# Kernel optimization log

Hardware: AMD Instinct MI355X
Metric: run time of the kernel (lower is better)

Reference implementation:

```python
import jax, jax.numpy as jnp
import numpy as np

N_NODES = 40000
N_EDGES = 640000
D = 128
N_GRAPHS = 64


def gcn_conv(x, W, b, edge_index):
    """PyG-style GCNConv: add self-loops, symmetric norm, linear, scatter-add."""
    n = x.shape[0]
    loops = jnp.arange(n, dtype=edge_index.dtype)
    src = jnp.concatenate([edge_index[0], loops])  # message sources (x_j)
    dst = jnp.concatenate([edge_index[1], loops])  # aggregation targets
    # deg computed over targets (col) with unit edge weights, incl. self-loops
    deg = jax.ops.segment_sum(jnp.ones_like(src, dtype=x.dtype), dst, num_segments=n)
    dinv = jnp.where(deg > 0, jax.lax.rsqrt(jnp.maximum(deg, 1.0)), 0.0)
    norm = dinv[src] * dinv[dst]  # [E+N]
    h = x @ W  # [N, d_out]
    out = jax.ops.segment_sum(norm[:, None] * h[src], dst, num_segments=n)
    return out + b


def global_mean_pool(x, batch, num_graphs):
    summed = jax.ops.segment_sum(x, batch, num_segments=num_graphs)
    counts = jax.ops.segment_sum(jnp.ones((x.shape[0],), x.dtype), batch, num_segments=num_graphs)
    return summed / jnp.maximum(counts, 1.0)[:, None]


def setup_inputs() -> dict:
    key = jax.random.key(0)
    ks = jax.random.split(key, 6)
    x = jax.random.normal(ks[0], (N_NODES, D), dtype=jnp.float32)
    edge_index = jax.random.randint(ks[1], (2, N_EDGES), 0, N_NODES)
    batch = jnp.sort(jax.random.randint(ks[2], (N_NODES,), 0, N_GRAPHS))
    s = 1.0 / np.sqrt(D)
    W1 = jax.random.normal(ks[3], (D, D), dtype=jnp.float32) * s
    W2 = jax.random.normal(ks[4], (D, D), dtype=jnp.float32) * s
    b1 = jnp.zeros((D,), jnp.float32)
    b2 = jnp.zeros((D,), jnp.float32)
    return {"x": x, "edge_index": edge_index, "batch": batch,
            "W1": W1, "b1": b1, "W2": W2, "b2": b2}


def reference(x, edge_index, batch, W1, b1, W2, b2):
    h = jax.nn.relu(gcn_conv(x, W1, b1, edge_index))
    h = gcn_conv(h, W2, b2, edge_index)  # no ReLU on last layer
    return global_mean_pool(h, batch, N_GRAPHS)
```

## Files before the change

kernel.cpp:

```cpp
#include <hip/hip_runtime.h>

#define D 128
#define N_GRAPHS 64

typedef unsigned int uint32;
typedef __attribute__((ext_vector_type(8))) _Float16 f16x8;
typedef __attribute__((ext_vector_type(4))) float f32x4;

__device__ __forceinline__ float hl(uint32 u) {
    return (float)__builtin_bit_cast(_Float16, (unsigned short)(u & 0xFFFF));
}
__device__ __forceinline__ float hh(uint32 u) {
    return (float)__builtin_bit_cast(_Float16, (unsigned short)(u >> 16));
}
__device__ __forceinline__ uint32 h2pair(float a, float b) {
    unsigned short ua = __builtin_bit_cast(unsigned short, (_Float16)a);
    unsigned short ub = __builtin_bit_cast(unsigned short, (_Float16)b);
    return (uint32)ua | ((uint32)ub << 16);
}

__global__ __launch_bounds__(256) void prep_kernel(int* __restrict__ cnt,
                                                   const float* __restrict__ W1,
                                                   uint32* __restrict__ Wh, int n) {
    int i = blockIdx.x * 256 + threadIdx.x;
    if (i < n) {
        cnt[i] = 0;
    } else if (i < n + D * (D / 2)) {
        int j = i - n;
        int nn = j & 127, kd = j >> 7;
        float v0 = W1[(size_t)(2 * kd) * D + nn];
        float v1 = W1[(size_t)(2 * kd + 1) * D + nn];
        Wh[nn * 64 + kd] = h2pair(v0, v1);
    }
}


#define GBM 64

__global__ __launch_bounds__(256) void count_gemm_kernel(
    const float* __restrict__ A, const uint32* __restrict__ Wh,
    uint32* __restrict__ hb, int M, int gemmBlocks,
    const int* __restrict__ dst, int* __restrict__ cnt,
    int* __restrict__ rank, int E) {
    __shared__ uint32 lds[64 * 68];

    if (blockIdx.x >= gemmBlocks) {
        int e = (blockIdx.x - gemmBlocks) * 256 + threadIdx.x;
        if (e < E) rank[e] = atomicAdd(&cnt[dst[e]], 1);
        return;
    }

    uint32* As = lds;
    int tid = threadIdx.x;
    int row0 = blockIdx.x * GBM;

#pragma unroll
    for (int j = 0; j < 8; ++j) {
        int idx = tid + j * 256;
        int r = idx >> 5, c4 = idx & 31;
        float4 v = make_float4(0.f, 0.f, 0.f, 0.f);
        if (row0 + r < M) v = *(const float4*)&A[(size_t)(row0 + r) * D + c4 * 4];
        As[r * 68 + c4 * 2 + 0] = h2pair(v.x, v.y);
        As[r * 68 + c4 * 2 + 1] = h2pair(v.z, v.w);
    }
    __syncthreads();

    int wave = tid >> 6, lane = tid & 63;
    int quad = lane >> 4, l16 = lane & 15;
    int wr = (wave & 1) * 32;
    int wc = (wave >> 1) * 64;
    f32x4 acc[2][4];
#pragma unroll
    for (int mi = 0; mi < 2; ++mi)
#pragma unroll
        for (int ni = 0; ni < 4; ++ni) acc[mi][ni] = (f32x4){0.f, 0.f, 0.f, 0.f};

#pragma unroll
    for (int ks = 0; ks < 4; ++ks) {
        int kd = ks * 16 + quad * 4;
        f16x8 a0 = *(f16x8*)&As[(wr + l16) * 68 + kd];
        f16x8 a1 = *(f16x8*)&As[(wr + 16 + l16) * 68 + kd];
        f16x8 b0 = *(const f16x8*)&Wh[(wc + l16) * 64 + kd];
        f16x8 b1 = *(const f16x8*)&Wh[(wc + 16 + l16) * 64 + kd];
        f16x8 b2 = *(const f16x8*)&Wh[(wc + 32 + l16) * 64 + kd];
        f16x8 b3 = *(const f16x8*)&Wh[(wc + 48 + l16) * 64 + kd];
        acc[0][0] = __builtin_amdgcn_mfma_f32_16x16x32_f16(a0, b0, acc[0][0], 0, 0, 0);
        acc[0][1] = __builtin_amdgcn_mfma_f32_16x16x32_f16(a0, b1, acc[0][1], 0, 0, 0);
        acc[0][2] = __builtin_amdgcn_mfma_f32_16x16x32_f16(a0, b2, acc[0][2], 0, 0, 0);
        acc[0][3] = __builtin_amdgcn_mfma_f32_16x16x32_f16(a0, b3, acc[0][3], 0, 0, 0);
        acc[1][0] = __builtin_amdgcn_mfma_f32_16x16x32_f16(a1, b0, acc[1][0], 0, 0, 0);
        acc[1][1] = __builtin_amdgcn_mfma_f32_16x16x32_f16(a1, b1, acc[1][1], 0, 0, 0);
        acc[1][2] = __builtin_amdgcn_mfma_f32_16x16x32_f16(a1, b2, acc[1][2], 0, 0, 0);
        acc[1][3] = __builtin_amdgcn_mfma_f32_16x16x32_f16(a1, b3, acc[1][3], 0, 0, 0);
    }
    __syncthreads();

    unsigned short* cs = (unsigned short*)lds;
#pragma unroll
    for (int mi = 0; mi < 2; ++mi)
#pragma unroll
        for (int ni = 0; ni < 4; ++ni)
#pragma unroll
            for (int r = 0; r < 4; ++r) {
                int row = wr + mi * 16 + quad * 4 + r;
                int col2 = wc + ni * 16 + l16;
                cs[row * 128 + col2] =
                    __builtin_bit_cast(unsigned short, (_Float16)acc[mi][ni][r]);
            }
    __syncthreads();
#pragma unroll
    for (int j = 0; j < 4; ++j) {
        int idx = tid + j * 256;
        int r = idx >> 4, q = idx & 15;
        if (row0 + r < M)
            *(uint4*)&hb[(size_t)(row0 + r) * 64 + q * 4] = *(uint4*)&lds[r * 64 + q * 4];
    }
}


__global__ __launch_bounds__(1024) void scanA_kernel(const int* __restrict__ cnt,
                                                     int* __restrict__ rowptr,
                                                     int* __restrict__ tot,
                                                     float* __restrict__ dinv, int n) {
    __shared__ int swave[16];
    int t = threadIdx.x;
    int lane = t & 63, wave = t >> 6;
    int i = blockIdx.x * 1024 + t;
    int orig = (i < n) ? cnt[i] : 0;
    int v = orig;
#pragma unroll
    for (int off = 1; off < 64; off <<= 1) {
        int u = __shfl_up(v, off, 64);
        if (lane >= off) v += u;
    }
    if (lane == 63) swave[wave] = v;
    __syncthreads();
    if (wave == 0) {
        int wv = (lane < 16) ? swave[lane] : 0;
#pragma unroll
        for (int off = 1; off < 16; off <<= 1) {
            int u = __shfl_up(wv, off, 64);
            if (lane >= off) wv += u;
        }
        if (lane < 16) swave[lane] = wv;
    }
    if (i < n) dinv[i] = rsqrtf((float)(orig + 1));
    __syncthreads();
    int incl = v + ((wave > 0) ? swave[wave - 1] : 0);
    if (i < n) rowptr[i] = incl - orig;
    if (t == 1023) tot[blockIdx.x] = incl;
}

__global__ __launch_bounds__(1024) void scanB_kernel(int* __restrict__ rowptr,
                                                     const int* __restrict__ tot,
                                                     int n, int nchunks) {
    __shared__ int soff;
    int b = blockIdx.x, t = threadIdx.x;
    if (t == 0) {
        int o = 0;
        for (int j = 0; j < b; ++j) o += tot[j];
        soff = o;
    }
    __syncthreads();
    int i = b * 1024 + t;
    if (i < n) rowptr[i] += soff;
    if (b == 0 && t == 0) {
        int o = 0;
        for (int j = 0; j < nchunks; ++j) o += tot[j];
        rowptr[n] = o;
    }
}

__global__ __launch_bounds__(256) void scale_fill_kernel(
    uint32* __restrict__ hb, const float* __restrict__ dinv, int scaleBlocks, int n,
    const int* __restrict__ src, const int* __restrict__ dst,
    const int* __restrict__ rowptr, const int* __restrict__ rank,
    int* __restrict__ col, int E) {
    if (blockIdx.x >= scaleBlocks) {
        int e = (blockIdx.x - scaleBlocks) * 256 + threadIdx.x;
        if (e < E) col[rowptr[dst[e]] + rank[e]] = src[e];
        return;
    }
    int idx = blockIdx.x * 256 + threadIdx.x;
    if (idx < n * 16) {
        int node = idx >> 4;
        float dv = dinv[node];
        uint4 v = ((uint4*)hb)[idx];
        v.x = h2pair(dv * hl(v.x), dv * hh(v.x));
        v.y = h2pair(dv * hl(v.y), dv * hh(v.y));
        v.z = h2pair(dv * hl(v.z), dv * hh(v.z));
        v.w = h2pair(dv * hl(v.w), dv * hh(v.w));
        ((uint4*)hb)[idx] = v;
    }
}


__global__ __launch_bounds__(128) void agg_kernel(const uint32* __restrict__ hb,
                                                  const int* __restrict__ rowptr,
                                                  const int* __restrict__ col,
                                                  const float* __restrict__ dinv,
                                                  const float* __restrict__ bias,
                                                  uint32* __restrict__ h1, int n) {
    int tid = threadIdx.x;
    int lane16 = tid & 15;
    int slot = tid >> 4;
    int node = blockIdx.x * 8 + slot;
    if (node >= n) return;
    const uint4* __restrict__ h4 = (const uint4*)hb;

    float di = dinv[node];
    uint4 su = h4[(size_t)node * 16 + lane16];
    float a0 = hl(su.x), a1 = hh(su.x), a2 = hl(su.y), a3 = hh(su.y);
    float a4 = hl(su.z), a5 = hh(su.z), a6 = hl(su.w), a7 = hh(su.w);

    int k = rowptr[node], end = rowptr[node + 1];
    for (; k + 8 <= end; k += 8) {
        uint4 v[8];
#pragma unroll
        for (int j = 0; j < 8; ++j) v[j] = h4[(size_t)col[k + j] * 16 + lane16];
#pragma unroll
        for (int j = 0; j < 8; ++j) {
            a0 += hl(v[j].x); a1 += hh(v[j].x);
            a2 += hl(v[j].y); a3 += hh(v[j].y);
            a4 += hl(v[j].z); a5 += hh(v[j].z);
            a6 += hl(v[j].w); a7 += hh(v[j].w);
        }
    }
    for (; k < end; ++k) {
        uint4 v = h4[(size_t)col[k] * 16 + lane16];
        a0 += hl(v.x); a1 += hh(v.x);
        a2 += hl(v.y); a3 += hh(v.y);
        a4 += hl(v.z); a5 += hh(v.z);
        a6 += hl(v.w); a7 += hh(v.w);
    }

    float4 b4a = ((const float4*)bias)[2 * lane16];
    float4 b4b = ((const float4*)bias)[2 * lane16 + 1];
    float r0 = fmaxf(fmaf(di, a0, b4a.x), 0.f);
    float r1 = fmaxf(fmaf(di, a1, b4a.y), 0.f);
    float r2 = fmaxf(fmaf(di, a2, b4a.z), 0.f);
    float r3 = fmaxf(fmaf(di, a3, b4a.w), 0.f);
    float r4 = fmaxf(fmaf(di, a4, b4b.x), 0.f);
    float r5 = fmaxf(fmaf(di, a5, b4b.y), 0.f);
    float r6 = fmaxf(fmaf(di, a6, b4b.z), 0.f);
    float r7 = fmaxf(fmaf(di, a7, b4b.w), 0.f);
    uint4 o;
    o.x = h2pair(di * r0, di * r1);
    o.y = h2pair(di * r2, di * r3);
    o.z = h2pair(di * r4, di * r5);
    o.w = h2pair(di * r6, di * r7);
    ((uint4*)h1)[(size_t)node * 16 + lane16] = o;
}


__global__ __launch_bounds__(128) void agg2_kernel(const uint32* __restrict__ h1,
                                                   const int* __restrict__ rowptr,
                                                   const int* __restrict__ col,
                                                   const float* __restrict__ dinv,
                                                   float* __restrict__ P2, int n) {
    int tid = threadIdx.x;
    int lane16 = tid & 15;
    int slot = tid >> 4;
    int node = blockIdx.x * 8 + slot;
    if (node >= n) return;
    const uint4* __restrict__ h4 = (const uint4*)h1;

    float di = dinv[node];
    uint4 su = h4[(size_t)node * 16 + lane16];
    float a0 = hl(su.x), a1 = hh(su.x), a2 = hl(su.y), a3 = hh(su.y);
    float a4 = hl(su.z), a5 = hh(su.z), a6 = hl(su.w), a7 = hh(su.w);

    int k = rowptr[node], end = rowptr[node + 1];
    for (; k + 8 <= end; k += 8) {
        uint4 v[8];
#pragma unroll
        for (int j = 0; j < 8; ++j) v[j] = h4[(size_t)col[k + j] * 16 + lane16];
#pragma unroll
        for (int j = 0; j < 8; ++j) {
            a0 += hl(v[j].x); a1 += hh(v[j].x);
            a2 += hl(v[j].y); a3 += hh(v[j].y);
            a4 += hl(v[j].z); a5 += hh(v[j].z);
            a6 += hl(v[j].w); a7 += hh(v[j].w);
        }
    }
    for (; k < end; ++k) {
        uint4 v = h4[(size_t)col[k] * 16 + lane16];
        a0 += hl(v.x); a1 += hh(v.x);
        a2 += hl(v.y); a3 += hh(v.y);
        a4 += hl(v.z); a5 += hh(v.z);
        a6 += hl(v.w); a7 += hh(v.w);
    }

    float* p = &P2[(size_t)node * D + lane16 * 8];
    *(float4*)&p[0] = make_float4(di * a0, di * a1, di * a2, di * a3);
    *(float4*)&p[4] = make_float4(di * a4, di * a5, di * a6, di * a7);
}

#define PSL 16

__global__ __launch_bounds__(128) void pool_kernel(const float* __restrict__ P2,
                                                   const int* __restrict__ batch,
                                                   float* __restrict__ Ppart, int n) {
    __shared__ int srange[2];
    int t = threadIdx.x;
    int g = blockIdx.x >> 4;
    int kslice = blockIdx.x & 15;
    if (t == 0) {
        int lo = 0, hi = n;
        while (lo < hi) { int mid = (lo + hi) >> 1; if (batch[mid] < g) lo = mid + 1; else hi = mid; }
        srange[0] = lo;
        int g1 = g + 1;
        lo = 0; hi = n;
        while (lo < hi) { int mid = (lo + hi) >> 1; if (batch[mid] < g1) lo = mid + 1; else hi = mid; }
        srange[1] = lo;
    }
    __syncthreads();
    int lb = srange[0], cntg = srange[1] - srange[0];
    int a = lb + (int)(((long long)cntg * kslice) >> 4);
    int b = lb + (int)(((long long)cntg * (kslice + 1)) >> 4);

    float s = 0.f;
    int node = a;
    for (; node + 4 <= b; node += 4) {
        float v0 = P2[(size_t)(node + 0) * D + t];
        float v1 = P2[(size_t)(node + 1) * D + t];
        float v2 = P2[(size_t)(node + 2) * D + t];
        float v3 = P2[(size_t)(node + 3) * D + t];
        s += (v0 + v1) + (v2 + v3);
    }
    for (; node < b; ++node) s += P2[(size_t)node * D + t];
    Ppart[(size_t)blockIdx.x * D + t] = s;
}

__global__ __launch_bounds__(256) void out_kernel(const float* __restrict__ Ppart,
                                                  const float* __restrict__ W2,
                                                  const float* __restrict__ b2,
                                                  const int* __restrict__ batch, int n,
                                                  float* __restrict__ out) {
    __shared__ float gs[D];
    __shared__ float part[2][D];
    __shared__ float srinv;
    int g = blockIdx.x, t = threadIdx.x;
    int f = t & 127, half = t >> 7;
    if (t == 0) {
        int lo = 0, hi = n;
        while (lo < hi) { int mid = (lo + hi) >> 1; if (batch[mid] < g) lo = mid + 1; else hi = mid; }
        int lb = lo;
        int g1 = g + 1;
        lo = 0; hi = n;
        while (lo < hi) { int mid = (lo + hi) >> 1; if (batch[mid] < g1) lo = mid + 1; else hi = mid; }
        int cg = lo - lb;
        srinv = (cg > 0) ? 1.0f / (float)cg : 0.0f;
    }
    float s = 0.f;
    int j0 = half * (PSL / 2);
#pragma unroll
    for (int j = j0; j < j0 + PSL / 2; ++j)
        s += Ppart[((size_t)g * PSL + j) * D + f];
    part[half][f] = s;
    __syncthreads();
    if (half == 0) gs[f] = part[0][f] + part[1][f];
    __syncthreads();
    float acc = 0.f;
    int k0 = half * (D / 2);
#pragma unroll 8
    for (int k = k0; k < k0 + D / 2; ++k) acc = fmaf(gs[k], W2[k * D + f], acc);
    part[half][f] = acc;
    __syncthreads();
    if (half == 0) {
        float a = part[0][f] + part[1][f];
        float r = srinv;
        out[g * D + f] = (r > 0.f) ? fmaf(a, r, b2[f]) : 0.f;
    }
}


extern "C" void kernel_launch(void* const* d_in, const int* in_sizes, int n_in,
                              void* d_out, int out_size, void* d_ws, size_t ws_size,
                              hipStream_t stream) {
    const float* x  = (const float*)d_in[0];
    const int*   ei = (const int*)d_in[1];
    const int*   batch = (const int*)d_in[2];
    const float* W1 = (const float*)d_in[3];
    const float* b1 = (const float*)d_in[4];
    const float* W2 = (const float*)d_in[5];
    const float* b2 = (const float*)d_in[6];
    float* out = (float*)d_out;

    const int n = in_sizes[2];
    const int E = in_sizes[1] / 2;
    const int* src = ei;
    const int* dst = ei + E;

    char* ws = (char*)d_ws;
    size_t off = 0;
    auto carve = [&](size_t bytes) {
        size_t o = off;
        off = (off + bytes + 255) & ~(size_t)255;
        return (void*)(ws + o);
    };
    int*    cnt    = (int*)carve((size_t)n * 4);
    int*    rowptr = (int*)carve((size_t)(n + 1) * 4);
    float*  dinv   = (float*)carve((size_t)n * 4);
    int*    col    = (int*)carve((size_t)E * 4);
    uint32* hb     = (uint32*)carve((size_t)n * D * 2);
    uint32* h1     = (uint32*)carve((size_t)n * D * 2);
    int*    tot    = (int*)carve(64 * 4);
    int*    rank   = (int*)carve((size_t)E * 4);
    uint32* Wh     = (uint32*)carve((size_t)D * (D / 2) * 4);
    float*  P2     = (float*)carve((size_t)n * D * 4);
    float*  Ppart  = (float*)hb;
    (void)ws_size;

    const int nchunks = (n + 1023) >> 10;

    prep_kernel<<<(n + D * (D / 2) + 255) / 256, 256, 0, stream>>>(cnt, W1, Wh, n);

    const int gemmBlocks = (n + GBM - 1) / GBM;
    const int countBlocks = (E + 255) / 256;
    count_gemm_kernel<<<gemmBlocks + countBlocks, 256, 0, stream>>>(
        x, Wh, hb, n, gemmBlocks, dst, cnt, rank, E);

    scanA_kernel<<<nchunks, 1024, 0, stream>>>(cnt, rowptr, tot, dinv, n);
    scanB_kernel<<<nchunks, 1024, 0, stream>>>(rowptr, tot, n, nchunks);
    const int scaleBlocks = (n * 16 + 255) / 256;
    const int fillBlocks = (E + 255) / 256;
    scale_fill_kernel<<<scaleBlocks + fillBlocks, 256, 0, stream>>>(
        hb, dinv, scaleBlocks, n, src, dst, rowptr, rank, col, E);

    agg_kernel<<<(n + 7) / 8, 128, 0, stream>>>(hb, rowptr, col, dinv, b1, h1, n);

    agg2_kernel<<<(n + 7) / 8, 128, 0, stream>>>(h1, rowptr, col, dinv, P2, n);
    pool_kernel<<<N_GRAPHS * PSL, 128, 0, stream>>>(P2, batch, Ppart, n);
    out_kernel<<<N_GRAPHS, 256, 0, stream>>>(Ppart, W2, b2, batch, n, out);
}
```

Baseline: 192.4 us.

## Build CSR with LDS-privatized range histograms instead of global atomics

Replaces the global per-edge atomicAdd counting and rank array with per-block shared-memory histograms over node ranges and edge slices, followed by a column scan that produces per-slice base offsets. The scatter pass reuses LDS atomics to place column indices. The aim is to avoid contended global atomics and the rank buffer traffic. In exchange, each histogram block rereads its full edge slice once per node range (four ranges), so dst is read several times, and a 64-slice partial array plus an extra scan kernel are added.

```diff
diff --git a/kernel.cpp b/kernel.cpp
--- a/kernel.cpp
+++ b/kernel.cpp
@@ -19,15 +19,14 @@
     return (uint32)ua | ((uint32)ub << 16);
 }
 
-__global__ __launch_bounds__(256) void prep_kernel(int* __restrict__ cnt,
-                                                   const float* __restrict__ W1,
-                                                   uint32* __restrict__ Wh, int n) {
+#define BPR 10240
+#define NSLICE 64
+
+__global__ __launch_bounds__(256) void prep_kernel(const float* __restrict__ W1,
+                                                   uint32* __restrict__ Wh) {
     int i = blockIdx.x * 256 + threadIdx.x;
-    if (i < n) {
-        cnt[i] = 0;
-    } else if (i < n + D * (D / 2)) {
-        int j = i - n;
-        int nn = j & 127, kd = j >> 7;
+    if (i < D * (D / 2)) {
+        int nn = i & 127, kd = i >> 7;
         float v0 = W1[(size_t)(2 * kd) * D + nn];
         float v1 = W1[(size_t)(2 * kd + 1) * D + nn];
         Wh[nn * 64 + kd] = h2pair(v0, v1);
@@ -37,16 +36,30 @@
 
 #define GBM 64
 
-__global__ __launch_bounds__(256) void count_gemm_kernel(
+__global__ __launch_bounds__(256) void hist_gemm_kernel(
     const float* __restrict__ A, const uint32* __restrict__ Wh,
     uint32* __restrict__ hb, int M, int gemmBlocks,
-    const int* __restrict__ dst, int* __restrict__ cnt,
-    int* __restrict__ rank, int E) {
-    __shared__ uint32 lds[64 * 68];
+    const int* __restrict__ dst, uint32* __restrict__ partial,
+    int n, int E, int esl) {
+    __shared__ uint32 lds[BPR];
 
     if (blockIdx.x >= gemmBlocks) {
-        int e = (blockIdx.x - gemmBlocks) * 256 + threadIdx.x;
-        if (e < E) rank[e] = atomicAdd(&cnt[dst[e]], 1);
+        int hid = blockIdx.x - gemmBlocks;
+        int r = hid / NSLICE, s = hid % NSLICE;
+        int tid = threadIdx.x;
+#pragma unroll
+        for (int i = tid; i < BPR; i += 256) lds[i] = 0;
+        __syncthreads();
+        int bin0 = r * BPR;
+        int bin1 = min(bin0 + BPR, n);
+        int e0 = s * esl, e1 = min(e0 + esl, E);
+        for (int e = e0 + tid; e < e1; e += 256) {
+            int d = dst[e];
+            if (d >= bin0 && d < bin1) atomicAdd(&lds[d - bin0], 1u);
+        }
+        __syncthreads();
+        for (int i = tid; i < bin1 - bin0; i += 256)
+            partial[(size_t)s * n + bin0 + i] = lds[i];
         return;
     }
 
@@ -117,6 +130,21 @@
     }
 }
 
+__global__ __launch_bounds__(1024) void colscan_kernel(uint32* __restrict__ partial,
+                                                       int* __restrict__ cnt, int n) {
+    int bin = blockIdx.x * 1024 + threadIdx.x;
+    if (bin >= n) return;
+    uint32 run = 0;
+#pragma unroll 8
+    for (int s = 0; s < NSLICE; ++s) {
+        size_t idx = (size_t)s * n + bin;
+        uint32 v = partial[idx];
+        partial[idx] = run;
+        run += v;
+    }
+    cnt[bin] = (int)run;
+}
+
 
 __global__ __launch_bounds__(1024) void scanA_kernel(const int* __restrict__ cnt,
                                                      int* __restrict__ rowptr,
@@ -171,17 +199,32 @@
     }
 }
 
-__global__ __launch_bounds__(256) void scale_fill_kernel(
-    uint32* __restrict__ hb, const float* __restrict__ dinv, int scaleBlocks, int n,
+__global__ __launch_bounds__(256) void scatter_scale_kernel(
+    uint32* __restrict__ hb, const float* __restrict__ dinv, int scatBlocks, int n,
     const int* __restrict__ src, const int* __restrict__ dst,
-    const int* __restrict__ rowptr, const int* __restrict__ rank,
-    int* __restrict__ col, int E) {
-    if (blockIdx.x >= scaleBlocks) {
-        int e = (blockIdx.x - scaleBlocks) * 256 + threadIdx.x;
-        if (e < E) col[rowptr[dst[e]] + rank[e]] = src[e];
+    const int* __restrict__ rowptr, const uint32* __restrict__ base,
+    int* __restrict__ col, int E, int esl) {
+    __shared__ uint32 run[BPR];
+    if (blockIdx.x < scatBlocks) {
+        int r = blockIdx.x / NSLICE, s = blockIdx.x % NSLICE;
+        int tid = threadIdx.x;
+#pragma unroll
+        for (int i = tid; i < BPR; i += 256) run[i] = 0;
+        __syncthreads();
+        int bin0 = r * BPR;
+        int bin1 = min(bin0 + BPR, n);
+        int e0 = s * esl, e1 = min(e0 + esl, E);
+        for (int e = e0 + tid; e < e1; e += 256) {
+            int d = dst[e];
+            if (d >= bin0 && d < bin1) {
+                uint32 lr = atomicAdd(&run[d - bin0], 1u);
+                int pos = rowptr[d] + (int)base[(size_t)s * n + d] + (int)lr;
+                col[pos] = src[e];
+            }
+        }
         return;
     }
-    int idx = blockIdx.x * 256 + threadIdx.x;
+    int idx = (blockIdx.x - scatBlocks) * 256 + threadIdx.x;
     if (idx < n * 16) {
         int node = idx >> 4;
         float dv = dinv[node];
@@ -251,7 +294,6 @@
     o.w = h2pair(di * r6, di * r7);
     ((uint4*)h1)[(size_t)node * 16 + lane16] = o;
 }
-
 
 __global__ __launch_bounds__(128) void agg2_kernel(const uint32* __restrict__ h1,
                                                    const int* __restrict__ rowptr,
@@ -406,27 +448,31 @@
     uint32* hb     = (uint32*)carve((size_t)n * D * 2);
     uint32* h1     = (uint32*)carve((size_t)n * D * 2);
     int*    tot    = (int*)carve(64 * 4);
-    int*    rank   = (int*)carve((size_t)E * 4);
+    uint32* partial= (uint32*)carve((size_t)NSLICE * n * 4);
     uint32* Wh     = (uint32*)carve((size_t)D * (D / 2) * 4);
     float*  P2     = (float*)carve((size_t)n * D * 4);
     float*  Ppart  = (float*)hb;
     (void)ws_size;
 
     const int nchunks = (n + 1023) >> 10;
-
-    prep_kernel<<<(n + D * (D / 2) + 255) / 256, 256, 0, stream>>>(cnt, W1, Wh, n);
+    const int nrange = (n + BPR - 1) / BPR;
+    const int esl = (E + NSLICE - 1) / NSLICE;
+
+    prep_kernel<<<(D * (D / 2) + 255) / 256, 256, 0, stream>>>(W1, Wh);
 
     const int gemmBlocks = (n + GBM - 1) / GBM;
-    const int countBlocks = (E + 255) / 256;
-    count_gemm_kernel<<<gemmBlocks + countBlocks, 256, 0, stream>>>(
-        x, Wh, hb, n, gemmBlocks, dst, cnt, rank, E);
+    const int histBlocks = nrange * NSLICE;
+    hist_gemm_kernel<<<gemmBlocks + histBlocks, 256, 0, stream>>>(
+        x, Wh, hb, n, gemmBlocks, dst, partial, n, E, esl);
+
+    colscan_kernel<<<nchunks, 1024, 0, stream>>>(partial, cnt, n);
 
     scanA_kernel<<<nchunks, 1024, 0, stream>>>(cnt, rowptr, tot, dinv, n);
     scanB_kernel<<<nchunks, 1024, 0, stream>>>(rowptr, tot, n, nchunks);
+    const int scatBlocks = nrange * NSLICE;
     const int scaleBlocks = (n * 16 + 255) / 256;
-    const int fillBlocks = (E + 255) / 256;
-    scale_fill_kernel<<<scaleBlocks + fillBlocks, 256, 0, stream>>>(
-        hb, dinv, scaleBlocks, n, src, dst, rowptr, rank, col, E);
+    scatter_scale_kernel<<<scatBlocks + scaleBlocks, 256, 0, stream>>>(
+        hb, dinv, scatBlocks, n, src, dst, rowptr, partial, col, E, esl);
 
     agg_kernel<<<(n + 7) / 8, 128, 0, stream>>>(hb, rowptr, col, dinv, b1, h1, n);
 
```

After: 208.0 us. 8.1% more time.
